# Kernel tuning notes

Hardware: AMD Instinct MI355X
Metric: run time of the kernel (lower is better)

The kernel has to match this reference:

```python
import jax, jax.numpy as jnp
import numpy as np

N_NODES = 50000
N_EDGES = 800000
D = 64          # encoder output dim (encoder.out)
MLP_DIM = 64    # mlp_edge_model hidden dim


def setup_inputs() -> dict:
    key = jax.random.key(0)
    ks = jax.random.split(key, 8)
    x = jax.random.normal(ks[0], (N_NODES, D), dtype=jnp.float32)
    edge_index = jax.random.randint(ks[1], (2, N_EDGES), 0, N_NODES, dtype=jnp.int64)
    # xavier-ish scaled weights
    W_enc = jax.random.normal(ks[2], (D, D), dtype=jnp.float32) * (1.0 / np.sqrt(D))
    b_enc = jnp.zeros((D,), dtype=jnp.float32)
    W1 = jax.random.normal(ks[3], (2 * D, MLP_DIM), dtype=jnp.float32) * (1.0 / np.sqrt(2 * D))
    b1 = jnp.zeros((MLP_DIM,), dtype=jnp.float32)
    W2 = jax.random.normal(ks[4], (MLP_DIM, 1), dtype=jnp.float32) * (1.0 / np.sqrt(MLP_DIM))
    b2 = jnp.zeros((1,), dtype=jnp.float32)
    return {"x": x, "edge_index": edge_index, "W_enc": W_enc, "b_enc": b_enc,
            "W1": W1, "b1": b1, "W2": W2, "b2": b2}


def reference(x, edge_index, W_enc, b_enc, W1, b1, W2, b2):
    src, dst = edge_index[0], edge_index[1]
    # --- encoder: 1-layer message-passing GCN stand-in ---
    agg = jax.ops.segment_sum(x[src], dst, num_segments=N_NODES)   # [N, D]
    node_emb = jax.nn.relu((x + agg) @ W_enc + b_enc)              # [N, D]
    # --- gather src/dst embeddings, concat, 2-layer MLP edge scorer ---
    edge_emb = jnp.concatenate([node_emb[src], node_emb[dst]], axis=1)  # [E, 2D]
    h = jax.nn.relu(edge_emb @ W1 + b1)                            # [E, mlp_dim]
    edge_logits = h @ W2 + b2                                      # [E, 1]
    return edge_logits
```

## Files before the change

kernel.cpp:

```cpp
#include <hip/hip_runtime.h>
#include <hip/hip_bf16.h>
#include <stdint.h>

#define N_NODES 50000
#define N_EDGES 800000
#define D 64
#define VROWS 50048
#define NBLK 196
#define CVT_BLOCKS 3125

typedef __hip_bfloat16 bf16;
typedef __bf16 bf16x8 __attribute__((ext_vector_type(8)));
typedef float  f32x4  __attribute__((ext_vector_type(4)));

__device__ __forceinline__ float bu2f(unsigned short u) {
    unsigned int w = ((unsigned int)u) << 16;
    return __builtin_bit_cast(float, w);
}
__device__ __forceinline__ unsigned short f2bu(float f) {
    bf16 h = __float2bfloat16(f);
    return __builtin_bit_cast(unsigned short, h);
}
__device__ __forceinline__ float ldf(const void* p, size_t i, bool f32mode) {
    if (f32mode) return ((const float*)p)[i];
    return bu2f(((const unsigned short*)p)[i]);
}
__device__ __forceinline__ void stf(void* p, size_t i, float v, bool f32mode) {
    if (f32mode) ((float*)p)[i] = v;
    else ((unsigned short*)p)[i] = f2bu(v);
}
__device__ __forceinline__ int ldidx(const int* ei, size_t e, int row, bool i64mode) {
    if (i64mode) return ei[((size_t)row * N_EDGES + e) * 2];
    return ei[(size_t)row * N_EDGES + e];
}
__device__ __forceinline__ void unpack8(uint4 v, float* f) {
    f[0] = bu2f(v.x & 0xffff); f[1] = bu2f(v.x >> 16);
    f[2] = bu2f(v.y & 0xffff); f[3] = bu2f(v.y >> 16);
    f[4] = bu2f(v.z & 0xffff); f[5] = bu2f(v.z >> 16);
    f[6] = bu2f(v.w & 0xffff); f[7] = bu2f(v.w >> 16);
}

__global__ __launch_bounds__(256) void init_kernel(
    const void* __restrict__ x, const int* __restrict__ ei,
    const void* __restrict__ W_enc, const void* __restrict__ b_enc,
    const void* __restrict__ W1,
    const void* __restrict__ W2, const void* __restrict__ b1,
    const void* __restrict__ b2,
    int* __restrict__ flags, unsigned short* __restrict__ w2bf,
    float* __restrict__ b1f, float* __restrict__ bencf,
    float* __restrict__ b2fp,
    int* __restrict__ counts,
    unsigned short* __restrict__ xbf,
    unsigned short* __restrict__ dst16, unsigned short* __restrict__ src16,
    unsigned short* __restrict__ wencbf, unsigned short* __restrict__ w1bf)
{
    __shared__ int sh_f32m, sh_i64m;
    int tid = threadIdx.x;

    if (tid < 64) {
        const unsigned short* u = (const unsigned short*)x;
        int weird = 0, zeros = 0;
        #pragma unroll
        for (int k = tid; k < 128; k += 64) {
            int ex = (u[2 * k] >> 7) & 0xFF;
            if (ex < 90 || ex > 160) ++weird;
            if (ei[2 * k + 1] == 0) ++zeros;
        }
        #pragma unroll
        for (int off = 1; off < 64; off <<= 1) {
            weird += __shfl_xor(weird, off, 64);
            zeros += __shfl_xor(zeros, off, 64);
        }
        if (tid == 0) {
            sh_f32m = (weird > 32) ? 1 : 0;
            sh_i64m = (zeros > 120) ? 1 : 0;
        }
    }
    __syncthreads();
    bool f32m = sh_f32m != 0;
    bool i64m = sh_i64m != 0;

    if (blockIdx.x == 0) {
        if (tid < 64) {
            w2bf[tid] = f2bu(ldf(W2, tid, f32m));
            b1f[tid]  = ldf(b1, tid, f32m);
            bencf[tid] = ldf(b_enc, tid, f32m);
        }
        if (tid == 0) {
            flags[0] = f32m ? 1 : 0;
            flags[1] = sh_i64m;
            b2fp[0] = ldf(b2, 0, f32m);
        }
    }
    if (blockIdx.x == 1) {
        for (int t = tid; t < 4096; t += 256)
            wencbf[t] = f2bu(ldf(W_enc, t, f32m));
        for (int t = tid; t < 8192; t += 256)
            w1bf[t] = f2bu(ldf(W1, t, f32m));
    }

    int cbase = blockIdx.x * 16 + (tid & 15);
    if (tid < 16 && cbase < N_NODES) counts[cbase] = 0;

    int e = blockIdx.x * 256 + tid;
    dst16[e] = (unsigned short)ldidx(ei, e, 1, i64m);
    src16[e] = (unsigned short)ldidx(ei, e, 0, i64m);

    size_t idx4 = (size_t)blockIdx.x * 256 + tid;
    if (f32m) {
        float4 fv = ((const float4*)x)[idx4];
        ushort4 o;
        o.x = f2bu(fv.x); o.y = f2bu(fv.y); o.z = f2bu(fv.z); o.w = f2bu(fv.w);
        ((ushort4*)xbf)[idx4] = o;
    } else {
        ((uint2*)xbf)[idx4] = ((const uint2*)x)[idx4];
    }
}

__global__ __launch_bounds__(256) void hist_kernel(
    const unsigned short* __restrict__ dst16, int* __restrict__ counts,
    unsigned short* __restrict__ rank)
{
    int grp = blockIdx.x & 7;
    int e = (blockIdx.x >> 3) * 256 + threadIdx.x;
    if (e >= N_EDGES) return;
    int d = dst16[e];
    if (((d >> 6) & 7) != grp) return;
    rank[e] = (unsigned short)atomicAdd(&counts[d], 1);
}

__global__ __launch_bounds__(256) void scan1_kernel(
    const int* __restrict__ counts, int* __restrict__ partials)
{
    int tid = threadIdx.x;
    int i = blockIdx.x * 256 + tid;
    int v = (i < N_NODES) ? counts[i] : 0;
    #pragma unroll
    for (int off = 1; off < 64; off <<= 1) v += __shfl_xor(v, off, 64);
    __shared__ int ws[4];
    if ((tid & 63) == 0) ws[tid >> 6] = v;
    __syncthreads();
    if (tid == 0) partials[blockIdx.x] = ws[0] + ws[1] + ws[2] + ws[3];
}

__global__ __launch_bounds__(256) void scan3_kernel(
    const int* __restrict__ counts, const int* __restrict__ partials,
    int* __restrict__ offsets)
{
    __shared__ int s[256];
    __shared__ int ws[4];
    int tid = threadIdx.x;
    int b   = blockIdx.x;

    int pv = (tid < b) ? partials[tid] : 0;
    #pragma unroll
    for (int off = 1; off < 64; off <<= 1) pv += __shfl_xor(pv, off, 64);
    if ((tid & 63) == 0) ws[tid >> 6] = pv;
    __syncthreads();
    int prefix = ws[0] + ws[1] + ws[2] + ws[3];

    int i = b * 256 + tid;
    int v = (i < N_NODES) ? counts[i] : 0;
    s[tid] = v;
    __syncthreads();
    for (int off = 1; off < 256; off <<= 1) {
        int t = (tid >= off) ? s[tid - off] : 0;
        __syncthreads();
        s[tid] += t;
        __syncthreads();
    }
    if (i < N_NODES) offsets[i] = prefix + s[tid] - v;
    if (b == NBLK - 1 && tid == 255) offsets[N_NODES] = prefix + s[255];
}

__global__ __launch_bounds__(256) void fill_kernel(
    const unsigned short* __restrict__ dst16,
    const unsigned short* __restrict__ src16,
    const int* __restrict__ offsets,
    const unsigned short* __restrict__ rank,
    unsigned short* __restrict__ sarr, int* __restrict__ earr)
{
    int e = blockIdx.x * 256 + threadIdx.x;
    if (e >= N_EDGES) return;
    int d = dst16[e];
    int pos = offsets[d] + (int)rank[e];
    sarr[pos] = src16[e];
    earr[pos] = e;
}

__global__ __launch_bounds__(256) void gather_kernel(
    const unsigned short* __restrict__ xbf,
    const int* __restrict__ offsets, const unsigned short* __restrict__ sarr,
    unsigned short* __restrict__ vtab)
{
    int w    = (blockIdx.x * 256 + threadIdx.x) >> 6;
    int lane = threadIdx.x & 63;
    if (w >= N_NODES) return;
    int beg = offsets[w], end = offsets[w + 1];
    int f8   = lane & 7;
    int slot = lane >> 3;

    float acc[8] = {0.f, 0.f, 0.f, 0.f, 0.f, 0.f, 0.f, 0.f};
    if (slot == 0) {
        uint4 q = ((const uint4*)xbf)[(size_t)w * 8 + f8];
        unpack8(q, acc);
    }

    int j = beg;
    for (; j + 16 <= end; j += 16) {
        int s0 = sarr[j + slot];
        int s1 = sarr[j + 8 + slot];
        uint4 q0 = ((const uint4*)xbf)[(size_t)s0 * 8 + f8];
        uint4 q1 = ((const uint4*)xbf)[(size_t)s1 * 8 + f8];
        float f0[8], f1[8];
        unpack8(q0, f0);
        unpack8(q1, f1);
        #pragma unroll
        for (int i = 0; i < 8; ++i) acc[i] += f0[i] + f1[i];
    }
    for (; j < end; j += 8) {
        int e = j + slot;
        bool ok = e < end;
        int s = sarr[ok ? e : beg];
        uint4 q = ((const uint4*)xbf)[(size_t)s * 8 + f8];
        float f[8];
        unpack8(q, f);
        if (ok) {
            #pragma unroll
            for (int i = 0; i < 8; ++i) acc[i] += f[i];
        }
    }

    #pragma unroll
    for (int i = 0; i < 8; ++i) {
        acc[i] += __shfl_xor(acc[i], 8, 64);
        acc[i] += __shfl_xor(acc[i], 16, 64);
        acc[i] += __shfl_xor(acc[i], 32, 64);
    }

    if (slot == 0) {
        uint4 o;
        o.x = (unsigned int)f2bu(acc[0]) | ((unsigned int)f2bu(acc[1]) << 16);
        o.y = (unsigned int)f2bu(acc[2]) | ((unsigned int)f2bu(acc[3]) << 16);
        o.z = (unsigned int)f2bu(acc[4]) | ((unsigned int)f2bu(acc[5]) << 16);
        o.w = (unsigned int)f2bu(acc[6]) | ((unsigned int)f2bu(acc[7]) << 16);
        ((uint4*)vtab)[(size_t)w * 8 + f8] = o;
    }
}

__global__ __launch_bounds__(256) void nodemm_kernel(
    const unsigned short* vtab,
    const unsigned short* __restrict__ wencbf,
    const unsigned short* __restrict__ w1bf,
    unsigned short* p_src, unsigned short* p_dst,
    const float* __restrict__ b1f, const float* __restrict__ bencf)
{
    __shared__ unsigned short wtWe[64 * 72];
    __shared__ unsigned short wtWa[64 * 72];
    __shared__ unsigned short wtWb[64 * 72];
    __shared__ float benc[64];
    __shared__ unsigned short ebuf[4][16 * 72];

    int tid = threadIdx.x;
    for (int t = tid; t < 4096; t += 256) {
        int i = t >> 6, j = t & 63;
        wtWe[j * 72 + i] = wencbf[t];
        wtWa[j * 72 + i] = w1bf[t];
        wtWb[j * 72 + i] = w1bf[4096 + t];
    }
    if (tid < 64) benc[tid] = bencf[tid];
    __syncthreads();

    int wave = tid >> 6;
    int lane = tid & 63;
    int lo   = lane & 15;
    int quad = lane >> 4;
    unsigned short* eb = ebuf[wave];
    int base = blockIdx.x * 64 + wave * 16;

    bf16x8 av0 = *(const bf16x8*)&vtab[(size_t)(base + lo) * D + quad * 8];
    bf16x8 av1 = *(const bf16x8*)&vtab[(size_t)(base + lo) * D + 32 + quad * 8];

    f32x4 z = {0.f, 0.f, 0.f, 0.f};
    f32x4 acc1[4] = {z, z, z, z};
    #pragma unroll
    for (int nt = 0; nt < 4; ++nt) {
        bf16x8 b0  = *(const bf16x8*)&wtWe[(nt * 16 + lo) * 72 + quad * 8];
        bf16x8 b1v = *(const bf16x8*)&wtWe[(nt * 16 + lo) * 72 + 32 + quad * 8];
        acc1[nt] = __builtin_amdgcn_mfma_f32_16x16x32_bf16(av0, b0, acc1[nt], 0, 0, 0);
        acc1[nt] = __builtin_amdgcn_mfma_f32_16x16x32_bf16(av1, b1v, acc1[nt], 0, 0, 0);
    }
    #pragma unroll
    for (int nt = 0; nt < 4; ++nt) {
        float bias = benc[nt * 16 + lo];
        #pragma unroll
        for (int r = 0; r < 4; ++r) {
            int m = quad * 4 + r;
            float ev = fmaxf(acc1[nt][r] + bias, 0.f);
            eb[m * 72 + nt * 16 + lo] = f2bu(ev);
        }
    }

    bf16x8 ae0 = *(const bf16x8*)&eb[lo * 72 + quad * 8];
    bf16x8 ae1 = *(const bf16x8*)&eb[lo * 72 + 32 + quad * 8];

    f32x4 acc2[4] = {z, z, z, z};
    f32x4 acc3[4] = {z, z, z, z};
    #pragma unroll
    for (int nt = 0; nt < 4; ++nt) {
        bf16x8 ba0 = *(const bf16x8*)&wtWa[(nt * 16 + lo) * 72 + quad * 8];
        bf16x8 ba1 = *(const bf16x8*)&wtWa[(nt * 16 + lo) * 72 + 32 + quad * 8];
        bf16x8 bb0 = *(const bf16x8*)&wtWb[(nt * 16 + lo) * 72 + quad * 8];
        bf16x8 bb1 = *(const bf16x8*)&wtWb[(nt * 16 + lo) * 72 + 32 + quad * 8];
        acc2[nt] = __builtin_amdgcn_mfma_f32_16x16x32_bf16(ae0, ba0, acc2[nt], 0, 0, 0);
        acc2[nt] = __builtin_amdgcn_mfma_f32_16x16x32_bf16(ae1, ba1, acc2[nt], 0, 0, 0);
        acc3[nt] = __builtin_amdgcn_mfma_f32_16x16x32_bf16(ae0, bb0, acc3[nt], 0, 0, 0);
        acc3[nt] = __builtin_amdgcn_mfma_f32_16x16x32_bf16(ae1, bb1, acc3[nt], 0, 0, 0);
    }
    #pragma unroll
    for (int nt = 0; nt < 4; ++nt) {
        float b1v = b1f[nt * 16 + lo];
        #pragma unroll
        for (int r = 0; r < 4; ++r) {
            int node = base + quad * 4 + r;
            if (node < N_NODES) {
                size_t idx = (size_t)node * D + nt * 16 + lo;
                p_src[idx] = f2bu(acc2[nt][r] + b1v);
                p_dst[idx] = f2bu(acc3[nt][r]);
            }
        }
    }
}

__global__ __launch_bounds__(256) void edge_kernel(
    const unsigned short* __restrict__ p_src,
    const unsigned short* __restrict__ p_dst,
    const int* __restrict__ offsets,
    const unsigned short* __restrict__ sarr, const int* __restrict__ earr,
    const unsigned short* __restrict__ w2bf, const float* __restrict__ b2fp,
    void* __restrict__ out, const int* __restrict__ flags)
{
    bool f32m = flags[0] != 0;
    int w    = (blockIdx.x * 256 + threadIdx.x) >> 6;
    int lane = threadIdx.x & 63;
    if (w >= N_NODES) return;
    int beg = offsets[w], end = offsets[w + 1];
    if (beg == end) return;

    int sub = lane & 7;
    int g   = lane >> 3;

    uint4 pdv = ((const uint4*)p_dst)[(size_t)w * 8 + sub];
    uint4 w2v = ((const uint4*)w2bf)[sub];
    float pd[8], w2[8];
    unpack8(pdv, pd);
    unpack8(w2v, w2);
    float bb = b2fp[0];

    int j = beg;
    for (; j + 16 <= end; j += 16) {
        int p0 = j + g, p1 = j + 8 + g;
        int s0 = sarr[p0];
        int s1 = sarr[p1];
        uint4 q0 = ((const uint4*)p_src)[(size_t)s0 * 8 + sub];
        uint4 q1 = ((const uint4*)p_src)[(size_t)s1 * 8 + sub];
        float f0[8], f1[8];
        unpack8(q0, f0);
        unpack8(q1, f1);
        float c0 = 0.f, c1 = 0.f;
        #pragma unroll
        for (int i = 0; i < 8; ++i) {
            c0 += fmaxf(f0[i] + pd[i], 0.f) * w2[i];
            c1 += fmaxf(f1[i] + pd[i], 0.f) * w2[i];
        }
        c0 += __shfl_xor(c0, 1, 64);
        c0 += __shfl_xor(c0, 2, 64);
        c0 += __shfl_xor(c0, 4, 64);
        c1 += __shfl_xor(c1, 1, 64);
        c1 += __shfl_xor(c1, 2, 64);
        c1 += __shfl_xor(c1, 4, 64);
        if (sub == 0) {
            stf(out, earr[p0], c0 + bb, f32m);
            stf(out, earr[p1], c1 + bb, f32m);
        }
    }
    for (; j < end; j += 8) {
        int pos = j + g;
        bool ok = pos < end;
        int idx = ok ? pos : beg;
        int s = sarr[idx];
        uint4 psv = ((const uint4*)p_src)[(size_t)s * 8 + sub];
        float ps[8];
        unpack8(psv, ps);
        float c = 0.f;
        #pragma unroll
        for (int i = 0; i < 8; ++i)
            c += fmaxf(ps[i] + pd[i], 0.f) * w2[i];
        c += __shfl_xor(c, 1, 64);
        c += __shfl_xor(c, 2, 64);
        c += __shfl_xor(c, 4, 64);
        if (sub == 0 && ok) {
            int eid = earr[pos];
            stf(out, eid, c + bb, f32m);
        }
    }
}

extern "C" void kernel_launch(void* const* d_in, const int* in_sizes, int n_in,
                              void* d_out, int out_size, void* d_ws, size_t ws_size,
                              hipStream_t stream)
{
    const void* x     = d_in[0];
    const int*  ei    = (const int*)d_in[1];
    const void* W_enc = d_in[2];
    const void* b_enc = d_in[3];
    const void* W1    = d_in[4];
    const void* b1    = d_in[5];
    const void* W2    = d_in[6];
    const void* b2    = d_in[7];

    const size_t NTv = (size_t)VROWS * D;
    unsigned short* p_src = (unsigned short*)d_ws;
    unsigned short* p_dst = p_src + NTv;
    unsigned short* xbf   = p_dst + NTv;
    unsigned short* sarr  = xbf + NTv;
    int*   earr    = (int*)(sarr + N_EDGES);
    float* b1f     = (float*)(earr + N_EDGES);
    unsigned short* w2bf = (unsigned short*)(b1f + 64);
    float* b2fp    = (float*)(w2bf + 64);
    int*   counts  = (int*)(b2fp + 4);
    int*   offsets = counts + N_NODES;
    unsigned short* rank = (unsigned short*)(offsets + N_NODES + 1);
    int*   flags   = (int*)(rank + N_EDGES);
    int*   partials = flags + 2;
    unsigned short* dst16 = (unsigned short*)(partials + NBLK);
    unsigned short* src16 = dst16 + N_EDGES;
    unsigned short* wencbf = src16 + N_EDGES;
    unsigned short* w1bf   = wencbf + 4096;
    float* bencf   = (float*)(w1bf + 8192);

    unsigned short* vtab = p_src;

    init_kernel<<<CVT_BLOCKS, 256, 0, stream>>>(
        x, ei, W_enc, b_enc, W1, W2, b1, b2,
        flags, w2bf, b1f, bencf, b2fp, counts, xbf,
        dst16, src16, wencbf, w1bf);

    const int EB  = (N_EDGES + 255) / 256;
    const int EB8 = EB * 8;
    hist_kernel<<<EB8, 256, 0, stream>>>(dst16, counts, rank);
    scan1_kernel<<<NBLK, 256, 0, stream>>>(counts, partials);
    scan3_kernel<<<NBLK, 256, 0, stream>>>(counts, partials, offsets);
    fill_kernel<<<EB, 256, 0, stream>>>(dst16, src16, offsets, rank, sarr, earr);

    const int NWB = (N_NODES * 64 + 255) / 256;
    gather_kernel<<<NWB, 256, 0, stream>>>(xbf, offsets, sarr, vtab);
    nodemm_kernel<<<(N_NODES + 63) / 64, 256, 0, stream>>>(vtab, wencbf, w1bf,
                                                           p_src, p_dst, b1f, bencf);
    edge_kernel<<<NWB, 256, 0, stream>>>(p_src, p_dst, offsets, sarr, earr,
                                         w2bf, b2fp, d_out, flags);
}
```

Baseline: 214.4 us.

## Fuse histogram, scan and fill into one cooperative kernel with grid syncs

Replaces four separate launches (hist, scan1, scan3, fill) with a single cooperative kernel that loops over virtual blocks and uses grid-wide syncs between phases. This removes three kernel launch boundaries and their drain/launch gaps. It adds grid.sync costs and needs all 1008 blocks resident at once. The hist phase loses parallelism because 25000 virtual blocks are now processed by 1008 persistent blocks.

```diff
diff --git a/kernel.cpp b/kernel.cpp
--- a/kernel.cpp
+++ b/kernel.cpp
@@ -1,6 +1,9 @@
 #include <hip/hip_runtime.h>
 #include <hip/hip_bf16.h>
+#include <hip/hip_cooperative_groups.h>
 #include <stdint.h>
+
+namespace cg = cooperative_groups;
 
 #define N_NODES 50000
 #define N_EDGES 800000
@@ -8,6 +11,9 @@
 #define VROWS 50048
 #define NBLK 196
 #define CVT_BLOCKS 3125
+#define EB 3125
+#define EB8 25000
+#define COOP_GRID 1008
 
 typedef __hip_bfloat16 bf16;
 typedef __bf16 bf16x8 __attribute__((ext_vector_type(8)));
@@ -117,75 +123,75 @@
     }
 }
 
-__global__ __launch_bounds__(256) void hist_kernel(
-    const unsigned short* __restrict__ dst16, int* __restrict__ counts,
-    unsigned short* __restrict__ rank)
-{
-    int grp = blockIdx.x & 7;
-    int e = (blockIdx.x >> 3) * 256 + threadIdx.x;
-    if (e >= N_EDGES) return;
-    int d = dst16[e];
-    if (((d >> 6) & 7) != grp) return;
-    rank[e] = (unsigned short)atomicAdd(&counts[d], 1);
-}
-
-__global__ __launch_bounds__(256) void scan1_kernel(
-    const int* __restrict__ counts, int* __restrict__ partials)
-{
-    int tid = threadIdx.x;
-    int i = blockIdx.x * 256 + tid;
-    int v = (i < N_NODES) ? counts[i] : 0;
-    #pragma unroll
-    for (int off = 1; off < 64; off <<= 1) v += __shfl_xor(v, off, 64);
-    __shared__ int ws[4];
-    if ((tid & 63) == 0) ws[tid >> 6] = v;
-    __syncthreads();
-    if (tid == 0) partials[blockIdx.x] = ws[0] + ws[1] + ws[2] + ws[3];
-}
-
-__global__ __launch_bounds__(256) void scan3_kernel(
-    const int* __restrict__ counts, const int* __restrict__ partials,
-    int* __restrict__ offsets)
-{
+__global__ __launch_bounds__(256, 4) void prep_coop_kernel(
+    const unsigned short* __restrict__ dst16,
+    const unsigned short* __restrict__ src16,
+    int* __restrict__ counts, unsigned short* __restrict__ rank,
+    int* __restrict__ partials, int* __restrict__ offsets,
+    unsigned short* __restrict__ sarr, int* __restrict__ earr)
+{
+    cg::grid_group grid = cg::this_grid();
     __shared__ int s[256];
     __shared__ int ws[4];
     int tid = threadIdx.x;
-    int b   = blockIdx.x;
-
-    int pv = (tid < b) ? partials[tid] : 0;
-    #pragma unroll
-    for (int off = 1; off < 64; off <<= 1) pv += __shfl_xor(pv, off, 64);
-    if ((tid & 63) == 0) ws[tid >> 6] = pv;
-    __syncthreads();
-    int prefix = ws[0] + ws[1] + ws[2] + ws[3];
-
-    int i = b * 256 + tid;
-    int v = (i < N_NODES) ? counts[i] : 0;
-    s[tid] = v;
-    __syncthreads();
-    for (int off = 1; off < 256; off <<= 1) {
-        int t = (tid >= off) ? s[tid - off] : 0;
+    const int GD = gridDim.x;
+
+    for (int vb = blockIdx.x; vb < EB8; vb += GD) {
+        int grp = vb & 7;
+        int e = (vb >> 3) * 256 + tid;
+        if (e < N_EDGES) {
+            int d = dst16[e];
+            if (((d >> 6) & 7) == grp)
+                rank[e] = (unsigned short)atomicAdd(&counts[d], 1);
+        }
+    }
+    grid.sync();
+
+    for (int vb = blockIdx.x; vb < NBLK; vb += GD) {
         __syncthreads();
-        s[tid] += t;
+        int i = vb * 256 + tid;
+        int v = (i < N_NODES) ? counts[i] : 0;
+        #pragma unroll
+        for (int off = 1; off < 64; off <<= 1) v += __shfl_xor(v, off, 64);
+        if ((tid & 63) == 0) ws[tid >> 6] = v;
         __syncthreads();
-    }
-    if (i < N_NODES) offsets[i] = prefix + s[tid] - v;
-    if (b == NBLK - 1 && tid == 255) offsets[N_NODES] = prefix + s[255];
-}
-
-__global__ __launch_bounds__(256) void fill_kernel(
-    const unsigned short* __restrict__ dst16,
-    const unsigned short* __restrict__ src16,
-    const int* __restrict__ offsets,
-    const unsigned short* __restrict__ rank,
-    unsigned short* __restrict__ sarr, int* __restrict__ earr)
-{
-    int e = blockIdx.x * 256 + threadIdx.x;
-    if (e >= N_EDGES) return;
-    int d = dst16[e];
-    int pos = offsets[d] + (int)rank[e];
-    sarr[pos] = src16[e];
-    earr[pos] = e;
+        if (tid == 0) partials[vb] = ws[0] + ws[1] + ws[2] + ws[3];
+    }
+    grid.sync();
+
+    for (int vb = blockIdx.x; vb < NBLK; vb += GD) {
+        __syncthreads();
+        int pv = (tid < vb) ? partials[tid] : 0;
+        #pragma unroll
+        for (int off = 1; off < 64; off <<= 1) pv += __shfl_xor(pv, off, 64);
+        if ((tid & 63) == 0) ws[tid >> 6] = pv;
+        __syncthreads();
+        int prefix = ws[0] + ws[1] + ws[2] + ws[3];
+
+        int i = vb * 256 + tid;
+        int v = (i < N_NODES) ? counts[i] : 0;
+        s[tid] = v;
+        __syncthreads();
+        for (int off = 1; off < 256; off <<= 1) {
+            int t = (tid >= off) ? s[tid - off] : 0;
+            __syncthreads();
+            s[tid] += t;
+            __syncthreads();
+        }
+        if (i < N_NODES) offsets[i] = prefix + s[tid] - v;
+        if (vb == NBLK - 1 && tid == 255) offsets[N_NODES] = prefix + s[255];
+    }
+    grid.sync();
+
+    for (int vb = blockIdx.x; vb < EB; vb += GD) {
+        int e = vb * 256 + tid;
+        if (e < N_EDGES) {
+            int d = dst16[e];
+            int pos = offsets[d] + (int)rank[e];
+            sarr[pos] = src16[e];
+            earr[pos] = e;
+        }
+    }
 }
 
 __global__ __launch_bounds__(256) void gather_kernel(
@@ -446,12 +452,15 @@
         flags, w2bf, b1f, bencf, b2fp, counts, xbf,
         dst16, src16, wencbf, w1bf);
 
-    const int EB  = (N_EDGES + 255) / 256;
-    const int EB8 = EB * 8;
-    hist_kernel<<<EB8, 256, 0, stream>>>(dst16, counts, rank);
-    scan1_kernel<<<NBLK, 256, 0, stream>>>(counts, partials);
-    scan3_kernel<<<NBLK, 256, 0, stream>>>(counts, partials, offsets);
-    fill_kernel<<<EB, 256, 0, stream>>>(dst16, src16, offsets, rank, sarr, earr);
+    {
+        void* kargs[] = {
+            (void*)&dst16, (void*)&src16, (void*)&counts, (void*)&rank,
+            (void*)&partials, (void*)&offsets, (void*)&sarr, (void*)&earr
+        };
+        hipLaunchCooperativeKernel((const void*)prep_coop_kernel,
+                                   dim3(COOP_GRID), dim3(256),
+                                   kargs, 0, stream);
+    }
 
     const int NWB = (N_NODES * 64 + 255) / 256;
     gather_kernel<<<NWB, 256, 0, stream>>>(xbf, offsets, sarr, vtab);
```

Result: slower. 526.7 us (+145.7%).
